# Kernel optimization log

Measured on AMD Instinct MI355X. Metric: run time of the kernel, lower is better.

The kernel has to match this reference:

```python
import jax, jax.numpy as jnp
import numpy as np

D_IN = 1024
D_OUT = 1024
D_BOT = 512


def setup_inputs() -> dict:
    key = jax.random.key(0)
    ks = jax.random.split(key, 16)
    B, Sq, Skv = 8, 2048, 2048

    def lin(k, fan_in, fan_out):
        kw, kb = jax.random.split(k)
        bound = 1.0 / np.sqrt(fan_in)
        W = jax.random.uniform(kw, (fan_in, fan_out), jnp.float32, -bound, bound)
        b = jax.random.uniform(kb, (fan_out,), jnp.float32, -bound, bound)
        return W, b

    W1, b1 = lin(ks[0], D_IN, D_IN)
    W2, b2 = lin(ks[1], D_IN, D_BOT)
    W3, b3 = lin(ks[2], D_BOT, D_IN)
    W4, b4 = lin(ks[3], D_IN, D_IN)
    Wq, bq = lin(ks[4], D_IN, D_OUT)
    Wk, bk = lin(ks[5], D_IN, D_OUT)
    Wv, bv = lin(ks[6], D_IN, D_OUT)

    x = jax.random.normal(ks[7], (B, Sq, D_IN), jnp.float32)
    y = jax.random.normal(ks[8], (B, Skv, D_IN), jnp.float32)
    return {
        "x": x, "y": y,
        "W1": W1, "b1": b1, "W2": W2, "b2": b2,
        "W3": W3, "b3": b3, "W4": W4, "b4": b4,
        "Wq": Wq, "bq": bq, "Wk": Wk, "bk": bk, "Wv": Wv, "bv": bv,
    }


def reference(x, y, W1, b1, W2, b2, W3, b3, W4, b4, Wq, bq, Wk, bk, Wv, bv):
    # 4-layer MLP with ReLU after every linear
    h = jax.nn.relu(x @ W1 + b1)
    h = jax.nn.relu(h @ W2 + b2)
    h = jax.nn.relu(h @ W3 + b3)
    h = jax.nn.relu(h @ W4 + b4)
    # cross-attention projections
    q = h @ Wq + bq          # [B, Sq, D_OUT]
    k = y @ Wk + bk          # [B, Skv, D_OUT]
    v = y @ Wv + bv          # [B, Skv, D_OUT]
    scale = 1.0 / jnp.sqrt(jnp.float32(q.shape[-1]))
    scores = jnp.einsum('bqd,bkd->bqk', q, k) * scale  # [B, Sq, Skv]
    attn_w = jax.nn.softmax(scores, axis=-1)
    out = jnp.einsum('bqk,bkd->bqd', attn_w, v)
    return out
```

## Files before the change

kernel.cpp:

```cpp
#include <hip/hip_runtime.h>
#include <stdint.h>


typedef __attribute__((ext_vector_type(8))) short bf16x8;
typedef __attribute__((ext_vector_type(4))) float f32x4;
typedef __attribute__((ext_vector_type(8))) unsigned short u16x8;

__device__ __forceinline__ float bf2f(unsigned short u) {
    return __uint_as_float(((unsigned int)u) << 16);
}
__device__ __forceinline__ unsigned short f2bf(float f) {
    unsigned int u = __float_as_uint(f);
    unsigned int r = (u + 0x7fffu + ((u >> 16) & 1u)) >> 16;
    return (unsigned short)r;
}

__device__ __forceinline__ void async16(const void* g, void* l) {
    __builtin_amdgcn_global_load_lds(
        (const __attribute__((address_space(1))) unsigned int*)g,
        (__attribute__((address_space(3))) unsigned int*)l,
        16, 0, 0);
}

__global__ __launch_bounds__(64) void detect_dtype(
    const unsigned short* __restrict__ w, int* __restrict__ flag)
{
    const int t = threadIdx.x;
    int cnt = 0;
    for (int i = t; i < 4096; i += 64) {
        const unsigned e = (w[i] >> 7) & 0xFF;
        cnt += (e >= 140) ? 1 : 0;
    }
#pragma unroll
    for (int off = 32; off; off >>= 1) cnt += __shfl_xor(cnt, off, 64);
    if (t == 0) flag[0] = (cnt >= 8) ? 1 : 0;
}

__global__ __launch_bounds__(256) void conv_bias_all(
    const void* b1, const void* b2, const void* b3, const void* b4,
    const void* bq, const void* bk, const void* bv,
    float* __restrict__ out, const int* __restrict__ flag)
{
    const int i = blockIdx.x * 256 + threadIdx.x;
    const int slot = i >> 10, idx = i & 1023;
    if (slot == 1 && idx >= 512) return;
    const void* src = (slot == 0) ? b1 : (slot == 1) ? b2 : (slot == 2) ? b3 :
                      (slot == 3) ? b4 : (slot == 4) ? bq : (slot == 5) ? bk : bv;
    out[i] = (*flag) ? ((const float*)src)[idx]
                     : bf2f(((const unsigned short*)src)[idx]);
}

__device__ __forceinline__ void wt_body(
    const void* in, unsigned short* out, int R, int C, int f)
{
    __shared__ unsigned short tile[32][33];
    const int bc = blockIdx.x * 32;
    const int br = blockIdx.y * 32;
    const int x = threadIdx.x & 31;
    const int y = threadIdx.x >> 5;
#pragma unroll
    for (int i = 0; i < 4; i++) {
        const int r = y + i * 8;
        unsigned short v;
        if (f) v = f2bf(((const float*)in)[(size_t)(br + r) * C + bc + x]);
        else   v = ((const unsigned short*)in)[(size_t)(br + r) * C + bc + x];
        tile[r][x] = v;
    }
    __syncthreads();
#pragma unroll
    for (int i = 0; i < 4; i++) {
        const int r = y + i * 8;
        out[(size_t)(bc + r) * R + br + x] = tile[x][r];
    }
}

__global__ __launch_bounds__(256) void conv_weight_t7(
    const void* i0, unsigned short* o0, const void* i1, unsigned short* o1,
    const void* i2, unsigned short* o2, const void* i3, unsigned short* o3,
    const void* i4, unsigned short* o4, const void* i5, unsigned short* o5,
    const void* i6, unsigned short* o6, const int* flag)
{
    const int z = blockIdx.z;
    if (z == 5) {
        if (blockIdx.x >= 16) return;
        wt_body(i5, o5, 1024, 512, *flag);
        return;
    }
    if (z == 6) {
        if (blockIdx.y >= 16) return;
        wt_body(i6, o6, 512, 1024, *flag);
        return;
    }
    const void* in = (z == 0) ? i0 : (z == 1) ? i1 : (z == 2) ? i2 : (z == 3) ? i3 : i4;
    unsigned short* out = (z == 0) ? o0 : (z == 1) ? o1 : (z == 2) ? o2 : (z == 3) ? o3 : o4;
    wt_body(in, out, 1024, 1024, *flag);
}

__global__ __launch_bounds__(256) void conv_to_bf16(
    const void* __restrict__ in, unsigned short* __restrict__ out,
    int n, const int* __restrict__ flag)
{
    const int i = (blockIdx.x * 256 + threadIdx.x) * 8;
    if (i >= n) return;
    if (*flag) {
        const float4* p = (const float4*)((const float*)in + i);
        const float4 a = p[0], b = p[1];
        u16x8 o;
        o[0] = f2bf(a.x); o[1] = f2bf(a.y); o[2] = f2bf(a.z); o[3] = f2bf(a.w);
        o[4] = f2bf(b.x); o[5] = f2bf(b.y); o[6] = f2bf(b.z); o[7] = f2bf(b.w);
        *(u16x8*)(out + i) = o;
    } else {
        *(u16x8*)(out + i) = *(const u16x8*)((const unsigned short*)in + i);
    }
}

__global__ __launch_bounds__(256) void write_out(
    const unsigned short* __restrict__ src, void* __restrict__ dst,
    int n, const int* __restrict__ flag)
{
    const int i = (blockIdx.x * 256 + threadIdx.x) * 8;
    if (i >= n) return;
    const u16x8 v = *(const u16x8*)(src + i);
    if (*flag) {
        float4 a, b;
        a.x = bf2f(v[0]); a.y = bf2f(v[1]); a.z = bf2f(v[2]); a.w = bf2f(v[3]);
        b.x = bf2f(v[4]); b.y = bf2f(v[5]); b.z = bf2f(v[6]); b.w = bf2f(v[7]);
        float4* p = (float4*)((float*)dst + i);
        p[0] = a; p[1] = b;
    } else {
        *(u16x8*)((unsigned short*)dst + i) = v;
    }
}

template <int RELU, int BIAS, int OUTF, int SWZ>
__global__ __launch_bounds__(256, 2) void gemm_bt(
    const unsigned short* __restrict__ A, const unsigned short* __restrict__ B,
    const float* __restrict__ bias, void* __restrict__ C,
    int M, int N, int K, float alpha,
    long long sA, long long sB, long long sC, const int* __restrict__ flag)
{
    int bxi = blockIdx.x, byi = blockIdx.y;
    if (SWZ) {
        const int id = byi * gridDim.x + bxi;
        bxi = (id >> 3) % gridDim.x;
        byi = (id >> 3) / gridDim.x * 8 + (id & 7);
    }
    const int z = blockIdx.z;
    A += (size_t)z * (size_t)sA;
    B += (size_t)z * (size_t)sB;
    const size_t cofs = (size_t)z * (size_t)sC;

    const int bm = byi * 128;
    const int bn = bxi * 128;
    const int t = threadIdx.x;
    const int lane = t & 63;
    const int w = t >> 6;
    const int wr = (w >> 1) * 64;
    const int wc = (w & 1) * 64;

    __shared__ unsigned short sAt[128 * 32];
    __shared__ unsigned short sBt[128 * 32];

    f32x4 acc[4][4];
#pragma unroll
    for (int i = 0; i < 4; i++)
#pragma unroll
        for (int j = 0; j < 4; j++)
            acc[i][j] = (f32x4){0.f, 0.f, 0.f, 0.f};

    const int tr = t >> 2;
    const int tc = (t & 3) << 3;
    const unsigned short* ga = A + (size_t)(bm + tr) * K + tc;
    const unsigned short* gb = B + (size_t)(bn + tr) * K + tc;
    unsigned short* la = &sAt[tr * 32 + tc];
    unsigned short* lb = &sBt[tr * 32 + tc];

    const int am = wr + (lane & 15);
    const int bn_ = wc + (lane & 15);
    const int ak = (lane >> 4) * 8;

    for (int k0 = 0; k0 < K; k0 += 32) {
        async16(ga, la);
        async16(ga + (size_t)64 * K, la + 64 * 32);
        async16(gb, lb);
        async16(gb + (size_t)64 * K, lb + 64 * 32);
        ga += 32;
        gb += 32;
        __syncthreads();

        bf16x8 af[4], bfr[4];
#pragma unroll
        for (int i = 0; i < 4; i++)
            af[i] = *(const bf16x8*)&sAt[(am + i * 16) * 32 + ak];
#pragma unroll
        for (int j = 0; j < 4; j++)
            bfr[j] = *(const bf16x8*)&sBt[(bn_ + j * 16) * 32 + ak];
#pragma unroll
        for (int i = 0; i < 4; i++)
#pragma unroll
            for (int j = 0; j < 4; j++)
                acc[i][j] = __builtin_amdgcn_mfma_f32_16x16x32_bf16(
                    af[i], bfr[j], acc[i][j], 0, 0, 0);
        __syncthreads();
    }

    const int fl = OUTF ? *flag : 0;
#pragma unroll
    for (int i = 0; i < 4; i++) {
        const int row0 = bm + wr + i * 16 + (lane >> 4) * 4;
#pragma unroll
        for (int j = 0; j < 4; j++) {
            const int col = bn + wc + j * 16 + (lane & 15);
            float bc = 0.f;
            if (BIAS == 1) bc = bias[col];
#pragma unroll
            for (int r = 0; r < 4; r++) {
                float bv = bc;
                if (BIAS == 2) bv = bias[row0 + r];
                float vv = acc[i][j][r] * alpha + bv;
                if (RELU) vv = fmaxf(vv, 0.f);
                const size_t idx = cofs + (size_t)(row0 + r) * N + col;
                if (OUTF && fl) ((float*)C)[idx] = vv;
                else ((unsigned short*)C)[idx] = f2bf(vv);
            }
        }
    }
}

#define G10_STG(SOFS, KOFS) do {                                               \
    async16(gAs + (KOFS), dA + (SOFS));                                        \
    async16(gAs + (KOFS) + rk128, dA + (SOFS) + 4096);                         \
    async16(gBs + (KOFS), dB + (SOFS));                                        \
    async16(gBs + (KOFS) + rk128, dB + (SOFS) + 4096);                         \
} while (0)

template <int RELU, int BIAS, int OUTF, int SWZ>
__global__ __launch_bounds__(512, 2) void gemm8(
    const unsigned short* __restrict__ A, const unsigned short* __restrict__ B,
    const float* __restrict__ bias, void* __restrict__ C,
    int M, int N, int K, float alpha,
    long long sA, long long sB, long long sC, const int* __restrict__ flag)
{
    extern __shared__ unsigned short lds[];
    (void)M;
    int bxi = blockIdx.x, byi = blockIdx.y;
    if (SWZ) {
        const int id = byi * gridDim.x + bxi;
        bxi = (id >> 3) % gridDim.x;
        byi = (id >> 3) / gridDim.x * 8 + (id & 7);
    }
    const int z = blockIdx.z;
    A += (size_t)z * (size_t)sA;
    B += (size_t)z * (size_t)sB;
    const size_t cofs = (size_t)z * (size_t)sC;

    const int bm = byi * 256;
    const int bn = bxi * 256;
    const int t = threadIdx.x;
    const int lane = t & 63;
    const int w = t >> 6;
    const int wm = w >> 2;
    const int wn = w & 3;

    const int soct = ((t & 3) ^ ((t >> 3) & 3)) << 3;
    const unsigned short* gAs = A + (size_t)(bm + (t >> 2)) * K + soct;
    const unsigned short* gBs = B + (size_t)(bn + (t >> 2)) * K + soct;
    const size_t rk128 = (size_t)128 * K;
    unsigned short* dA = lds + t * 8;
    unsigned short* dB = lds + 32768 + t * 8;

    const int l15 = lane & 15;
    const int oct = (((lane >> 4) ^ ((lane >> 1) & 3)) << 3);
    const int aoff = (wm * 128 + l15) * 32 + oct;
    const int boff = (wn * 64 + l15) * 32 + oct;

    f32x4 acc[8][4];
#pragma unroll
    for (int i = 0; i < 8; i++)
#pragma unroll
        for (int j = 0; j < 4; j++)
            acc[i][j] = (f32x4){0.f, 0.f, 0.f, 0.f};

    G10_STG(0, 0);
    G10_STG(8192, 32);
    asm volatile("s_waitcnt vmcnt(4)" ::: "memory");
    __builtin_amdgcn_s_barrier();
    asm volatile("" ::: "memory");

    const int NT = K >> 5;
    for (int T = 0; T < NT; ++T) {
        if (T + 2 < NT) {
            const int so = ((T + 2) & 3) * 8192;
            const int ko = (T + 2) << 5;
            G10_STG(so, ko);
        }
        const int sr = (T & 3) * 8192;
        const unsigned short* pa = lds + sr + aoff;
        const unsigned short* pb = lds + 32768 + sr + boff;
        bf16x8 bb[4], a[8];
#pragma unroll
        for (int n = 0; n < 4; n++)
            bb[n] = *(const bf16x8*)(pb + n * 512);
#pragma unroll
        for (int m = 0; m < 8; m++)
            a[m] = *(const bf16x8*)(pa + m * 512);
        __builtin_amdgcn_s_setprio(1);
#pragma unroll
        for (int m = 0; m < 8; m++)
#pragma unroll
            for (int n = 0; n < 4; n++)
                acc[m][n] = __builtin_amdgcn_mfma_f32_16x16x32_bf16(
                    a[m], bb[n], acc[m][n], 0, 0, 0);
        __builtin_amdgcn_s_setprio(0);
        if (T + 1 < NT) {
            if (T + 2 < NT) {
                asm volatile("s_waitcnt vmcnt(4)" ::: "memory");
            } else {
                asm volatile("s_waitcnt vmcnt(0)" ::: "memory");
            }
            __builtin_amdgcn_s_barrier();
            asm volatile("" ::: "memory");
        }
    }

    const int fl = OUTF ? *flag : 0;
#pragma unroll
    for (int mi = 0; mi < 8; mi++) {
        const int row0 = bm + wm * 128 + mi * 16 + (lane >> 4) * 4;
#pragma unroll
        for (int n = 0; n < 4; n++) {
            const int col = bn + wn * 64 + n * 16 + (lane & 15);
            float bc = 0.f;
            if (BIAS == 1) bc = bias[col];
#pragma unroll
            for (int r = 0; r < 4; r++) {
                float bv = bc;
                if (BIAS == 2) bv = bias[row0 + r];
                float vv = acc[mi][n][r] * alpha + bv;
                if (RELU) vv = fmaxf(vv, 0.f);
                const size_t idx = cofs + (size_t)(row0 + r) * N + col;
                if (OUTF && fl) ((float*)C)[idx] = vv;
                else ((unsigned short*)C)[idx] = f2bf(vv);
            }
        }
    }
}

__global__ __launch_bounds__(256) void softmax_rows(unsigned short* S, int n)
{
    const size_t row = blockIdx.x;
    unsigned short* p = S + row * (size_t)n;
    const int t = threadIdx.x;
    const int lane = t & 63;
    const int wave = t >> 6;

    u16x8 v = *(const u16x8*)(p + t * 8);
    float f[8];
    float m = -3.0e38f;
#pragma unroll
    for (int i = 0; i < 8; i++) {
        f[i] = bf2f(v[i]);
        m = fmaxf(m, f[i]);
    }
#pragma unroll
    for (int off = 32; off; off >>= 1) m = fmaxf(m, __shfl_xor(m, off, 64));
    __shared__ float redm[4];
    if (lane == 0) redm[wave] = m;
    __syncthreads();
    m = fmaxf(fmaxf(redm[0], redm[1]), fmaxf(redm[2], redm[3]));

    float e[8];
    float s = 0.f;
#pragma unroll
    for (int i = 0; i < 8; i++) {
        e[i] = __expf(f[i] - m);
        s += e[i];
    }
#pragma unroll
    for (int off = 32; off; off >>= 1) s += __shfl_xor(s, off, 64);
    __shared__ float reds[4];
    if (lane == 0) reds[wave] = s;
    __syncthreads();
    s = reds[0] + reds[1] + reds[2] + reds[3];
    const float inv = 1.0f / s;

    u16x8 o;
#pragma unroll
    for (int i = 0; i < 8; i++) o[i] = f2bf(e[i] * inv);
    *(u16x8*)(p + t * 8) = o;
}

extern "C" void kernel_launch(void* const* d_in, const int* in_sizes, int n_in,
                              void* d_out, int out_size, void* d_ws, size_t ws_size,
                              hipStream_t stream)
{
    const void* x  = d_in[0];
    const void* y  = d_in[1];
    const void* W1 = d_in[2];
    const void* b1 = d_in[3];
    const void* W2 = d_in[4];
    const void* b2 = d_in[5];
    const void* W3 = d_in[6];
    const void* b3 = d_in[7];
    const void* W4 = d_in[8];
    const void* b4 = d_in[9];
    const void* Wq = d_in[10];
    const void* bq = d_in[11];
    const void* Wk = d_in[12];
    const void* bk = d_in[13];
    const void* Wv = d_in[14];
    const void* bv = d_in[15];

    int* flag = (int*)d_ws;
    float* fb = (float*)((char*)d_ws + 64);
    unsigned short* arena = (unsigned short*)((char*)d_ws + 64 + 7 * 1024 * 4);
    const size_t baseB = 64 + 7 * 1024 * 4;
    const size_t MEG = 1024ull * 1024ull;

    auto needB = [&](int G, bool direct) -> size_t {
        return baseB + 2ull * ((6 + 16 + (size_t)G * 6 + (direct ? 0 : 16)) * MEG);
    };
    int G; bool direct;
    if (ws_size >= needB(8, true))      { G = 8; direct = true;  }
    else if (ws_size >= needB(4, false)) { G = 4; direct = false; }
    else if (ws_size >= needB(2, false)) { G = 2; direct = false; }
    else                                 { G = 1; direct = false; }

    unsigned short* W1t = arena;
    unsigned short* W2t = W1t + 1 * MEG;
    unsigned short* W3t = W2t + MEG / 2;
    unsigned short* W4t = W3t + MEG / 2;
    unsigned short* Wqt = W4t + 1 * MEG;
    unsigned short* Wkt = Wqt + 1 * MEG;
    unsigned short* Wvt = Wkt + 1 * MEG;
    unsigned short* XC  = Wvt + 1 * MEG;
    unsigned short* VT  = XC + 16 * MEG;
    unsigned short* SBUF = VT + (size_t)G * 2 * MEG;
    unsigned short* OUTS = SBUF + (size_t)G * 4 * MEG;

    unsigned short* PA = (unsigned short*)d_out;
    unsigned short* PB = PA + 16 * MEG;

    float* fb1 = fb;
    float* fb2 = fb + 1024;
    float* fb3 = fb + 2048;
    float* fb4 = fb + 3072;
    float* fbq = fb + 4096;
    float* fbk = fb + 5120;
    float* fbv = fb + 6144;

    const dim3 blk(256);
    const dim3 blk8(512);
    const int LDS8 = 131072;
    const int NE = 16 * 1024 * 1024;
    const int Mx = 16384;
    const long long Z0 = 0;
    const long long sQK = 2048ll * 1024;
    const long long sS  = 2048ll * 2048;

    (void)hipFuncSetAttribute((const void*)&gemm8<1, 1, 0, 1>,
                              hipFuncAttributeMaxDynamicSharedMemorySize, LDS8);
    (void)hipFuncSetAttribute((const void*)&gemm8<0, 1, 0, 1>,
                              hipFuncAttributeMaxDynamicSharedMemorySize, LDS8);
    (void)hipFuncSetAttribute((const void*)&gemm8<0, 2, 0, 0>,
                              hipFuncAttributeMaxDynamicSharedMemorySize, LDS8);
    (void)hipFuncSetAttribute((const void*)&gemm8<0, 0, 0, 1>,
                              hipFuncAttributeMaxDynamicSharedMemorySize, LDS8);
    (void)hipFuncSetAttribute((const void*)&gemm8<0, 0, 1, 1>,
                              hipFuncAttributeMaxDynamicSharedMemorySize, LDS8);

    detect_dtype<<<1, 64, 0, stream>>>((const unsigned short*)W1, flag);
    conv_bias_all<<<28, blk, 0, stream>>>(b1, b2, b3, b4, bq, bk, bv, fb, flag);
    conv_weight_t7<<<dim3(32, 32, 7), blk, 0, stream>>>(
        W1, W1t, W4, W4t, Wq, Wqt, Wk, Wkt, Wv, Wvt, W2, W2t, W3, W3t, flag);

    conv_to_bf16<<<8192, blk, 0, stream>>>(x, XC, NE, flag);

    gemm8<1, 1, 0, 1><<<dim3(4, 64), blk8, LDS8, stream>>>(
        XC, W1t, fb1, PA, Mx, 1024, 1024, 1.f, Z0, Z0, Z0, flag);
    gemm_bt<1, 1, 0, 1><<<dim3(4, 128), blk, 0, stream>>>(
        PA, W2t, fb2, PB, Mx, 512, 1024, 1.f, Z0, Z0, Z0, flag);
    gemm8<1, 1, 0, 1><<<dim3(4, 64), blk8, LDS8, stream>>>(
        PB, W3t, fb3, PA, Mx, 1024, 512, 1.f, Z0, Z0, Z0, flag);
    gemm8<1, 1, 0, 1><<<dim3(4, 64), blk8, LDS8, stream>>>(
        PA, W4t, fb4, PB, Mx, 1024, 1024, 1.f, Z0, Z0, Z0, flag);

    gemm8<0, 1, 0, 1><<<dim3(4, 64), blk8, LDS8, stream>>>(
        PB, Wqt, fbq, PA, Mx, 1024, 1024, 1.f, Z0, Z0, Z0, flag);
    conv_to_bf16<<<8192, blk, 0, stream>>>(y, XC, NE, flag);
    gemm8<0, 1, 0, 1><<<dim3(4, 64), blk8, LDS8, stream>>>(
        XC, Wkt, fbk, PB, Mx, 1024, 1024, 1.f, Z0, Z0, Z0, flag);

    if (direct) {
        gemm8<0, 2, 0, 0><<<dim3(8, 4, 8), blk8, LDS8, stream>>>(
            Wvt, XC, fbv, VT, 1024, 2048, 1024, 1.f, Z0, sQK, sQK, flag);
        gemm8<0, 0, 0, 1><<<dim3(8, 8, 8), blk8, LDS8, stream>>>(
            PA, PB, nullptr, SBUF, 2048, 2048, 1024, 0.03125f, sQK, sQK, sS, flag);
        softmax_rows<<<dim3(8 * 2048), blk, 0, stream>>>(SBUF, 2048);
        gemm8<0, 0, 1, 1><<<dim3(4, 8, 8), blk8, LDS8, stream>>>(
            SBUF, VT, nullptr, d_out, 2048, 1024, 2048, 1.f, sS, sQK, sQK, flag);
    } else {
        for (int g = 0; g < 8; g += G) {
            const size_t off = (size_t)g * 2048 * 1024;
            gemm_bt<0, 2, 0, 0><<<dim3(16, 8, G), blk, 0, stream>>>(
                Wvt, XC + off, fbv, VT, 1024, 2048, 1024, 1.f, Z0, sQK, sQK, flag);
            gemm_bt<0, 0, 0, 1><<<dim3(16, 16, G), blk, 0, stream>>>(
                PA + off, PB + off, nullptr, SBUF, 2048, 2048, 1024, 0.03125f, sQK, sQK, sS, flag);
            softmax_rows<<<dim3(G * 2048), blk, 0, stream>>>(SBUF, 2048);
            gemm_bt<0, 0, 0, 1><<<dim3(8, 16, G), blk, 0, stream>>>(
                SBUF, VT, nullptr, OUTS + off, 2048, 1024, 2048, 1.f, sS, sQK, sQK, flag);
        }
        write_out<<<8192, blk, 0, stream>>>(OUTS, d_out, NE, flag);
    }
}
```

Measured before the change: 606.0 us.

## Add 128x512-tile triple-buffered GEMM for projections and compute V via transpose

Introduces gemm_bt5, a 512-thread GEMM with 128x512 output tiles, a three-stage async LDS pipeline and smaller LDS (120KB), and uses it for the MLP layers and Q/K projections. The V projection is now computed as a standard row-major GEMM with column bias into a scratch buffer, followed by a new tiled transpose kernel that produces VT. The aim is better operand reuse and pipelining for the large M=16384 projections. The cost is an extra transpose pass and scratch buffer traffic, plus higher register pressure from the 4x8 accumulator layout.

```diff
diff --git a/kernel.cpp b/kernel.cpp
--- a/kernel.cpp
+++ b/kernel.cpp
@@ -94,6 +94,31 @@
     const void* in = (z == 0) ? i0 : (z == 1) ? i1 : (z == 2) ? i2 : (z == 3) ? i3 : i4;
     unsigned short* out = (z == 0) ? o0 : (z == 1) ? o1 : (z == 2) ? o2 : (z == 3) ? o3 : o4;
     wt_body(in, out, 1024, 1024, *flag);
+}
+
+__global__ __launch_bounds__(256) void transpose_bf16(
+    const unsigned short* __restrict__ in, unsigned short* __restrict__ out,
+    int R, int C)
+{
+    __shared__ unsigned short tile[32][33];
+    const size_t zofs = (size_t)blockIdx.z * R * C;
+    const unsigned short* ip = in + zofs;
+    unsigned short* op = out + zofs;
+    const int bc = blockIdx.x * 32;
+    const int br = blockIdx.y * 32;
+    const int x = threadIdx.x & 31;
+    const int y = threadIdx.x >> 5;
+#pragma unroll
+    for (int i = 0; i < 4; i++) {
+        const int r = y + i * 8;
+        tile[r][x] = ip[(size_t)(br + r) * C + bc + x];
+    }
+    __syncthreads();
+#pragma unroll
+    for (int i = 0; i < 4; i++) {
+        const int r = y + i * 8;
+        op[(size_t)(bc + r) * R + br + x] = tile[x][r];
+    }
 }
 
 __global__ __launch_bounds__(256) void conv_to_bf16(
@@ -330,6 +355,133 @@
 #pragma unroll
         for (int n = 0; n < 4; n++) {
             const int col = bn + wn * 64 + n * 16 + (lane & 15);
+            float bc = 0.f;
+            if (BIAS == 1) bc = bias[col];
+#pragma unroll
+            for (int r = 0; r < 4; r++) {
+                float bv = bc;
+                if (BIAS == 2) bv = bias[row0 + r];
+                float vv = acc[mi][n][r] * alpha + bv;
+                if (RELU) vv = fmaxf(vv, 0.f);
+                const size_t idx = cofs + (size_t)(row0 + r) * N + col;
+                if (OUTF && fl) ((float*)C)[idx] = vv;
+                else ((unsigned short*)C)[idx] = f2bf(vv);
+            }
+        }
+    }
+}
+
+template <int RELU, int BIAS, int OUTF, int SWZ>
+__global__ __launch_bounds__(512, 2) void gemm_bt5(
+    const unsigned short* __restrict__ A, const unsigned short* __restrict__ B,
+    const float* __restrict__ bias, void* __restrict__ C,
+    int M, int N, int K, float alpha,
+    long long sA, long long sB, long long sC, const int* __restrict__ flag)
+{
+    extern __shared__ unsigned short lds[];
+    (void)M;
+    int bxi = blockIdx.x, byi = blockIdx.y;
+    if (SWZ) {
+        const int id = byi * gridDim.x + bxi;
+        bxi = (id >> 3) % gridDim.x;
+        byi = (id >> 3) / gridDim.x * 8 + (id & 7);
+    }
+    const int z = blockIdx.z;
+    A += (size_t)z * (size_t)sA;
+    B += (size_t)z * (size_t)sB;
+    const size_t cofs = (size_t)z * (size_t)sC;
+
+    const int bm = byi * 128;
+    const int bn = bxi * 512;
+    const int t = threadIdx.x;
+    const int lane = t & 63;
+    const int w = t >> 6;
+    const int wm = w >> 2;
+    const int wn = w & 3;
+
+    const int soct = ((t & 3) ^ ((t >> 3) & 3)) << 3;
+    const unsigned short* gAs = A + (size_t)(bm + (t >> 2)) * K + soct;
+    const unsigned short* gBs = B + (size_t)(bn + (t >> 2)) * K + soct;
+    const size_t rk128 = (size_t)128 * K;
+    unsigned short* dA = lds + t * 8;
+    unsigned short* dB = lds + 12288 + t * 8;
+
+    const int l15 = lane & 15;
+    const int oct = (((lane >> 4) ^ ((lane >> 1) & 3)) << 3);
+    const int aoff = (wm * 64 + l15) * 32 + oct;
+    const int boff = (wn * 128 + l15) * 32 + oct;
+
+    f32x4 acc[4][8];
+#pragma unroll
+    for (int i = 0; i < 4; i++)
+#pragma unroll
+        for (int j = 0; j < 8; j++)
+            acc[i][j] = (f32x4){0.f, 0.f, 0.f, 0.f};
+
+    async16(gAs, dA);
+    async16(gBs, dB);
+    async16(gBs + rk128, dB + 4096);
+    async16(gBs + 2 * rk128, dB + 8192);
+    async16(gBs + 3 * rk128, dB + 12288);
+    async16(gAs + 32, dA + 4096);
+    async16(gBs + 32, dB + 16384);
+    async16(gBs + 32 + rk128, dB + 16384 + 4096);
+    async16(gBs + 32 + 2 * rk128, dB + 16384 + 8192);
+    async16(gBs + 32 + 3 * rk128, dB + 16384 + 12288);
+    asm volatile("s_waitcnt vmcnt(5)" ::: "memory");
+    __builtin_amdgcn_s_barrier();
+    asm volatile("" ::: "memory");
+
+    const int NT = K >> 5;
+    int rs = 0, ws = 2;
+    for (int T = 0; T < NT; ++T) {
+        if (T + 2 < NT) {
+            const int ko = (T + 2) << 5;
+            const int wa = ws * 4096;
+            const int wb = ws * 16384;
+            async16(gAs + ko, dA + wa);
+            async16(gBs + ko, dB + wb);
+            async16(gBs + ko + rk128, dB + wb + 4096);
+            async16(gBs + ko + 2 * rk128, dB + wb + 8192);
+            async16(gBs + ko + 3 * rk128, dB + wb + 12288);
+        }
+        const unsigned short* pa = lds + rs * 4096 + aoff;
+        const unsigned short* pb = lds + 12288 + rs * 16384 + boff;
+        bf16x8 a[4], bb[8];
+#pragma unroll
+        for (int m = 0; m < 4; m++)
+            a[m] = *(const bf16x8*)(pa + m * 512);
+#pragma unroll
+        for (int n = 0; n < 8; n++)
+            bb[n] = *(const bf16x8*)(pb + n * 512);
+        __builtin_amdgcn_s_setprio(1);
+#pragma unroll
+        for (int m = 0; m < 4; m++)
+#pragma unroll
+            for (int n = 0; n < 8; n++)
+                acc[m][n] = __builtin_amdgcn_mfma_f32_16x16x32_bf16(
+                    a[m], bb[n], acc[m][n], 0, 0, 0);
+        __builtin_amdgcn_s_setprio(0);
+        if (T + 1 < NT) {
+            if (T + 2 < NT) {
+                asm volatile("s_waitcnt vmcnt(5)" ::: "memory");
+            } else {
+                asm volatile("s_waitcnt vmcnt(0)" ::: "memory");
+            }
+            __builtin_amdgcn_s_barrier();
+            asm volatile("" ::: "memory");
+        }
+        rs = (rs == 2) ? 0 : rs + 1;
+        ws = (ws == 2) ? 0 : ws + 1;
+    }
+
+    const int fl = OUTF ? *flag : 0;
+#pragma unroll
+    for (int mi = 0; mi < 4; mi++) {
+        const int row0 = bm + wm * 64 + mi * 16 + (lane >> 4) * 4;
+#pragma unroll
+        for (int n = 0; n < 8; n++) {
+            const int col = bn + wn * 128 + n * 16 + (lane & 15);
             float bc = 0.f;
             if (BIAS == 1) bc = bias[col];
 #pragma unroll
@@ -452,18 +604,17 @@
     const dim3 blk(256);
     const dim3 blk8(512);
     const int LDS8 = 131072;
+    const int LDS5 = 122880;
     const int NE = 16 * 1024 * 1024;
     const int Mx = 16384;
     const long long Z0 = 0;
     const long long sQK = 2048ll * 1024;
     const long long sS  = 2048ll * 2048;
 
-    (void)hipFuncSetAttribute((const void*)&gemm8<1, 1, 0, 1>,
-                              hipFuncAttributeMaxDynamicSharedMemorySize, LDS8);
-    (void)hipFuncSetAttribute((const void*)&gemm8<0, 1, 0, 1>,
-                              hipFuncAttributeMaxDynamicSharedMemorySize, LDS8);
-    (void)hipFuncSetAttribute((const void*)&gemm8<0, 2, 0, 0>,
-                              hipFuncAttributeMaxDynamicSharedMemorySize, LDS8);
+    (void)hipFuncSetAttribute((const void*)&gemm_bt5<1, 1, 0, 1>,
+                              hipFuncAttributeMaxDynamicSharedMemorySize, LDS5);
+    (void)hipFuncSetAttribute((const void*)&gemm_bt5<0, 1, 0, 1>,
+                              hipFuncAttributeMaxDynamicSharedMemorySize, LDS5);
     (void)hipFuncSetAttribute((const void*)&gemm8<0, 0, 0, 1>,
                               hipFuncAttributeMaxDynamicSharedMemorySize, LDS8);
     (void)hipFuncSetAttribute((const void*)&gemm8<0, 0, 1, 1>,
@@ -476,24 +627,25 @@
 
     conv_to_bf16<<<8192, blk, 0, stream>>>(x, XC, NE, flag);
 
-    gemm8<1, 1, 0, 1><<<dim3(4, 64), blk8, LDS8, stream>>>(
+    gemm_bt5<1, 1, 0, 1><<<dim3(2, 128), blk8, LDS5, stream>>>(
         XC, W1t, fb1, PA, Mx, 1024, 1024, 1.f, Z0, Z0, Z0, flag);
     gemm_bt<1, 1, 0, 1><<<dim3(4, 128), blk, 0, stream>>>(
         PA, W2t, fb2, PB, Mx, 512, 1024, 1.f, Z0, Z0, Z0, flag);
-    gemm8<1, 1, 0, 1><<<dim3(4, 64), blk8, LDS8, stream>>>(
+    gemm_bt5<1, 1, 0, 1><<<dim3(2, 128), blk8, LDS5, stream>>>(
         PB, W3t, fb3, PA, Mx, 1024, 512, 1.f, Z0, Z0, Z0, flag);
-    gemm8<1, 1, 0, 1><<<dim3(4, 64), blk8, LDS8, stream>>>(
+    gemm_bt5<1, 1, 0, 1><<<dim3(2, 128), blk8, LDS5, stream>>>(
         PA, W4t, fb4, PB, Mx, 1024, 1024, 1.f, Z0, Z0, Z0, flag);
 
-    gemm8<0, 1, 0, 1><<<dim3(4, 64), blk8, LDS8, stream>>>(
+    gemm_bt5<0, 1, 0, 1><<<dim3(2, 128), blk8, LDS5, stream>>>(
         PB, Wqt, fbq, PA, Mx, 1024, 1024, 1.f, Z0, Z0, Z0, flag);
     conv_to_bf16<<<8192, blk, 0, stream>>>(y, XC, NE, flag);
-    gemm8<0, 1, 0, 1><<<dim3(4, 64), blk8, LDS8, stream>>>(
+    gemm_bt5<0, 1, 0, 1><<<dim3(2, 128), blk8, LDS5, stream>>>(
         XC, Wkt, fbk, PB, Mx, 1024, 1024, 1.f, Z0, Z0, Z0, flag);
 
     if (direct) {
-        gemm8<0, 2, 0, 0><<<dim3(8, 4, 8), blk8, LDS8, stream>>>(
-            Wvt, XC, fbv, VT, 1024, 2048, 1024, 1.f, Z0, sQK, sQK, flag);
+        gemm_bt5<0, 1, 0, 1><<<dim3(2, 128), blk8, LDS5, stream>>>(
+            XC, Wvt, fbv, SBUF, Mx, 1024, 1024, 1.f, Z0, Z0, Z0, flag);
+        transpose_bf16<<<dim3(32, 64, 8), blk, 0, stream>>>(SBUF, VT, 2048, 1024);
         gemm8<0, 0, 0, 1><<<dim3(8, 8, 8), blk8, LDS8, stream>>>(
             PA, PB, nullptr, SBUF, 2048, 2048, 1024, 0.03125f, sQK, sQK, sS, flag);
         softmax_rows<<<dim3(8 * 2048), blk, 0, stream>>>(SBUF, 2048);
```

New measurement: 637.8 us. +5.2%, slower.

## Fuse softmax into QK^T and PV GEMMs via row max/sum statistics

Applied to the files above, without the earlier changes.

Removes the separate softmax pass over the 8x2048x2048 score matrix. The QK^T GEMM now stores log2-scaled raw scores and emits per-tile row max and sum partials. A small reduce kernel merges these into a row max and inverse sum. The PV GEMM then exponentiates the A operand on the fly after the LDS load and scales its output by the inverse sum. It also switches the W2 layer from gemm_bt to the larger gemm8 tile. The cost is extra exp and bf16 conversion work inside the PV GEMM's inner loop, plus a workspace-size condition for the fused path.

```diff
diff --git a/kernel.cpp b/kernel.cpp
--- a/kernel.cpp
+++ b/kernel.cpp
@@ -5,6 +5,9 @@
 typedef __attribute__((ext_vector_type(8))) short bf16x8;
 typedef __attribute__((ext_vector_type(4))) float f32x4;
 typedef __attribute__((ext_vector_type(8))) unsigned short u16x8;
+
+#define LOG2E_F 1.44269504088896f
+#define LN2_F   0.69314718055995f
 
 __device__ __forceinline__ float bf2f(unsigned short u) {
     return __uint_as_float(((unsigned int)u) << 16);
@@ -234,15 +237,15 @@
     async16(gBs + (KOFS) + rk128, dB + (SOFS) + 4096);                         \
 } while (0)
 
-template <int RELU, int BIAS, int OUTF, int SWZ>
+template <int RELU, int BIAS, int OUTF, int SWZ, int STAT, int NORM>
 __global__ __launch_bounds__(512, 2) void gemm8(
     const unsigned short* __restrict__ A, const unsigned short* __restrict__ B,
     const float* __restrict__ bias, void* __restrict__ C,
     int M, int N, int K, float alpha,
-    long long sA, long long sB, long long sC, const int* __restrict__ flag)
+    long long sA, long long sB, long long sC, const int* __restrict__ flag,
+    const float* __restrict__ ms, float* __restrict__ ps)
 {
     extern __shared__ unsigned short lds[];
-    (void)M;
     int bxi = blockIdx.x, byi = blockIdx.y;
     if (SWZ) {
         const int id = byi * gridDim.x + bxi;
@@ -274,6 +277,15 @@
     const int aoff = (wm * 128 + l15) * 32 + oct;
     const int boff = (wn * 64 + l15) * 32 + oct;
 
+    float Mm[8];
+    if (NORM) {
+#pragma unroll
+        for (int m = 0; m < 8; m++) {
+            const int row = bm + wm * 128 + m * 16 + l15;
+            Mm[m] = ms[((size_t)z * M + row) * 2];
+        }
+    }
+
     f32x4 acc[8][4];
 #pragma unroll
     for (int i = 0; i < 8; i++)
@@ -304,6 +316,20 @@
 #pragma unroll
         for (int m = 0; m < 8; m++)
             a[m] = *(const bf16x8*)(pa + m * 512);
+        if (NORM) {
+#pragma unroll
+            for (int m = 0; m < 8; m++) {
+                bf16x8 v = a[m];
+                u16x8 o;
+#pragma unroll
+                for (int e = 0; e < 8; e++) {
+                    const float x = bf2f((unsigned short)v[e]);
+                    const float p = __expf((x - Mm[m]) * LN2_F);
+                    o[e] = f2bf(p);
+                }
+                a[m] = *(bf16x8*)&o;
+            }
+        }
         __builtin_amdgcn_s_setprio(1);
 #pragma unroll
         for (int m = 0; m < 8; m++)
@@ -327,9 +353,15 @@
 #pragma unroll
     for (int mi = 0; mi < 8; mi++) {
         const int row0 = bm + wm * 128 + mi * 16 + (lane >> 4) * 4;
+        float isv[4];
+        if (NORM) {
+#pragma unroll
+            for (int r = 0; r < 4; r++)
+                isv[r] = ms[((size_t)z * M + row0 + r) * 2 + 1];
+        }
 #pragma unroll
         for (int n = 0; n < 4; n++) {
-            const int col = bn + wn * 64 + n * 16 + (lane & 15);
+            const int col = bn + wn * 64 + n * 16 + l15;
             float bc = 0.f;
             if (BIAS == 1) bc = bias[col];
 #pragma unroll
@@ -337,6 +369,7 @@
                 float bv = bc;
                 if (BIAS == 2) bv = bias[row0 + r];
                 float vv = acc[mi][n][r] * alpha + bv;
+                if (NORM) vv *= isv[r];
                 if (RELU) vv = fmaxf(vv, 0.f);
                 const size_t idx = cofs + (size_t)(row0 + r) * N + col;
                 if (OUTF && fl) ((float*)C)[idx] = vv;
@@ -344,6 +377,64 @@
             }
         }
     }
+
+    if (STAT) {
+        __syncthreads();
+        float2* sl = (float2*)lds;
+#pragma unroll
+        for (int mi = 0; mi < 8; mi++) {
+#pragma unroll
+            for (int r = 0; r < 4; r++) {
+                float vr[4];
+#pragma unroll
+                for (int n = 0; n < 4; n++)
+                    vr[n] = bf2f(f2bf(acc[mi][n][r] * alpha));
+                float mx = fmaxf(fmaxf(vr[0], vr[1]), fmaxf(vr[2], vr[3]));
+#pragma unroll
+                for (int msk = 1; msk <= 8; msk <<= 1)
+                    mx = fmaxf(mx, __shfl_xor(mx, msk, 64));
+                float sm = 0.f;
+#pragma unroll
+                for (int n = 0; n < 4; n++)
+                    sm += __expf((vr[n] - mx) * LN2_F);
+#pragma unroll
+                for (int msk = 1; msk <= 8; msk <<= 1)
+                    sm += __shfl_xor(sm, msk, 64);
+                if (l15 == 0) {
+                    const int rl = wm * 128 + mi * 16 + (lane >> 4) * 4 + r;
+                    sl[rl * 4 + wn] = (float2){mx, sm};
+                }
+            }
+        }
+        __syncthreads();
+        if (t < 256) {
+            const float2 p0 = sl[t * 4 + 0], p1 = sl[t * 4 + 1];
+            const float2 p2 = sl[t * 4 + 2], p3 = sl[t * 4 + 3];
+            float Mx = fmaxf(fmaxf(p0.x, p1.x), fmaxf(p2.x, p3.x));
+            float S = p0.y * __expf((p0.x - Mx) * LN2_F)
+                    + p1.y * __expf((p1.x - Mx) * LN2_F)
+                    + p2.y * __expf((p2.x - Mx) * LN2_F)
+                    + p3.y * __expf((p3.x - Mx) * LN2_F);
+            float2* o = (float2*)ps;
+            o[((size_t)z * M + bm + t) * 8 + bxi] = (float2){Mx, S};
+        }
+    }
+}
+
+__global__ __launch_bounds__(256) void stats_reduce(
+    const float* __restrict__ ps, float* __restrict__ ms)
+{
+    const int i = blockIdx.x * 256 + threadIdx.x;
+    const float2* p = (const float2*)ps + (size_t)i * 8;
+    float M = p[0].x;
+#pragma unroll
+    for (int j = 1; j < 8; j++) M = fmaxf(M, p[j].x);
+    float S = 0.f;
+#pragma unroll
+    for (int j = 0; j < 8; j++)
+        S += p[j].y * __expf((p[j].x - M) * LN2_F);
+    float2* o = (float2*)ms;
+    o[i] = (float2){M, 1.0f / S};
 }
 
 __global__ __launch_bounds__(256) void softmax_rows(unsigned short* S, int n)
@@ -458,15 +549,23 @@
     const long long sQK = 2048ll * 1024;
     const long long sS  = 2048ll * 2048;
 
-    (void)hipFuncSetAttribute((const void*)&gemm8<1, 1, 0, 1>,
+    const bool fused = direct && (ws_size >= needB(8, true) + 2ull * MEG);
+    float* pstats = (float*)OUTS;
+    float* mstats = pstats + 8 * 2048 * 8 * 2;
+
+    (void)hipFuncSetAttribute((const void*)&gemm8<1, 1, 0, 1, 0, 0>,
                               hipFuncAttributeMaxDynamicSharedMemorySize, LDS8);
-    (void)hipFuncSetAttribute((const void*)&gemm8<0, 1, 0, 1>,
+    (void)hipFuncSetAttribute((const void*)&gemm8<0, 1, 0, 1, 0, 0>,
                               hipFuncAttributeMaxDynamicSharedMemorySize, LDS8);
-    (void)hipFuncSetAttribute((const void*)&gemm8<0, 2, 0, 0>,
+    (void)hipFuncSetAttribute((const void*)&gemm8<0, 2, 0, 0, 0, 0>,
                               hipFuncAttributeMaxDynamicSharedMemorySize, LDS8);
-    (void)hipFuncSetAttribute((const void*)&gemm8<0, 0, 0, 1>,
+    (void)hipFuncSetAttribute((const void*)&gemm8<0, 0, 0, 1, 0, 0>,
                               hipFuncAttributeMaxDynamicSharedMemorySize, LDS8);
-    (void)hipFuncSetAttribute((const void*)&gemm8<0, 0, 1, 1>,
+    (void)hipFuncSetAttribute((const void*)&gemm8<0, 0, 1, 1, 0, 0>,
+                              hipFuncAttributeMaxDynamicSharedMemorySize, LDS8);
+    (void)hipFuncSetAttribute((const void*)&gemm8<0, 0, 0, 1, 1, 0>,
+                              hipFuncAttributeMaxDynamicSharedMemorySize, LDS8);
+    (void)hipFuncSetAttribute((const void*)&gemm8<0, 0, 1, 1, 0, 1>,
                               hipFuncAttributeMaxDynamicSharedMemorySize, LDS8);
 
     detect_dtype<<<1, 64, 0, stream>>>((const unsigned short*)W1, flag);
@@ -476,29 +575,41 @@
 
     conv_to_bf16<<<8192, blk, 0, stream>>>(x, XC, NE, flag);
 
-    gemm8<1, 1, 0, 1><<<dim3(4, 64), blk8, LDS8, stream>>>(
-        XC, W1t, fb1, PA, Mx, 1024, 1024, 1.f, Z0, Z0, Z0, flag);
-    gemm_bt<1, 1, 0, 1><<<dim3(4, 128), blk, 0, stream>>>(
-        PA, W2t, fb2, PB, Mx, 512, 1024, 1.f, Z0, Z0, Z0, flag);
-    gemm8<1, 1, 0, 1><<<dim3(4, 64), blk8, LDS8, stream>>>(
-        PB, W3t, fb3, PA, Mx, 1024, 512, 1.f, Z0, Z0, Z0, flag);
-    gemm8<1, 1, 0, 1><<<dim3(4, 64), blk8, LDS8, stream>>>(
-        PA, W4t, fb4, PB, Mx, 1024, 1024, 1.f, Z0, Z0, Z0, flag);
-
-    gemm8<0, 1, 0, 1><<<dim3(4, 64), blk8, LDS8, stream>>>(
-        PB, Wqt, fbq, PA, Mx, 1024, 1024, 1.f, Z0, Z0, Z0, flag);
+    gemm8<1, 1, 0, 1, 0, 0><<<dim3(4, 64), blk8, LDS8, stream>>>(
+        XC, W1t, fb1, PA, Mx, 1024, 1024, 1.f, Z0, Z0, Z0, flag, nullptr, nullptr);
+    gemm8<1, 1, 0, 1, 0, 0><<<dim3(2, 64), blk8, LDS8, stream>>>(
+        PA, W2t, fb2, PB, Mx, 512, 1024, 1.f, Z0, Z0, Z0, flag, nullptr, nullptr);
+    gemm8<1, 1, 0, 1, 0, 0><<<dim3(4, 64), blk8, LDS8, stream>>>(
+        PB, W3t, fb3, PA, Mx, 1024, 512, 1.f, Z0, Z0, Z0, flag, nullptr, nullptr);
+    gemm8<1, 1, 0, 1, 0, 0><<<dim3(4, 64), blk8, LDS8, stream>>>(
+        PA, W4t, fb4, PB, Mx, 1024, 1024, 1.f, Z0, Z0, Z0, flag, nullptr, nullptr);
+
+    gemm8<0, 1, 0, 1, 0, 0><<<dim3(4, 64), blk8, LDS8, stream>>>(
+        PB, Wqt, fbq, PA, Mx, 1024, 1024, 1.f, Z0, Z0, Z0, flag, nullptr, nullptr);
     conv_to_bf16<<<8192, blk, 0, stream>>>(y, XC, NE, flag);
-    gemm8<0, 1, 0, 1><<<dim3(4, 64), blk8, LDS8, stream>>>(
-        XC, Wkt, fbk, PB, Mx, 1024, 1024, 1.f, Z0, Z0, Z0, flag);
+    gemm8<0, 1, 0, 1, 0, 0><<<dim3(4, 64), blk8, LDS8, stream>>>(
+        XC, Wkt, fbk, PB, Mx, 1024, 1024, 1.f, Z0, Z0, Z0, flag, nullptr, nullptr);
 
     if (direct) {
-        gemm8<0, 2, 0, 0><<<dim3(8, 4, 8), blk8, LDS8, stream>>>(
-            Wvt, XC, fbv, VT, 1024, 2048, 1024, 1.f, Z0, sQK, sQK, flag);
-        gemm8<0, 0, 0, 1><<<dim3(8, 8, 8), blk8, LDS8, stream>>>(
-            PA, PB, nullptr, SBUF, 2048, 2048, 1024, 0.03125f, sQK, sQK, sS, flag);
-        softmax_rows<<<dim3(8 * 2048), blk, 0, stream>>>(SBUF, 2048);
-        gemm8<0, 0, 1, 1><<<dim3(4, 8, 8), blk8, LDS8, stream>>>(
-            SBUF, VT, nullptr, d_out, 2048, 1024, 2048, 1.f, sS, sQK, sQK, flag);
+        gemm8<0, 2, 0, 0, 0, 0><<<dim3(8, 4, 8), blk8, LDS8, stream>>>(
+            Wvt, XC, fbv, VT, 1024, 2048, 1024, 1.f, Z0, sQK, sQK, flag, nullptr, nullptr);
+        if (fused) {
+            gemm8<0, 0, 0, 1, 1, 0><<<dim3(8, 8, 8), blk8, LDS8, stream>>>(
+                PA, PB, nullptr, SBUF, 2048, 2048, 1024, 0.03125f * LOG2E_F,
+                sQK, sQK, sS, flag, nullptr, pstats);
+            stats_reduce<<<64, blk, 0, stream>>>(pstats, mstats);
+            gemm8<0, 0, 1, 1, 0, 1><<<dim3(4, 8, 8), blk8, LDS8, stream>>>(
+                SBUF, VT, nullptr, d_out, 2048, 1024, 2048, 1.f,
+                sS, sQK, sQK, flag, mstats, nullptr);
+        } else {
+            gemm8<0, 0, 0, 1, 0, 0><<<dim3(8, 8, 8), blk8, LDS8, stream>>>(
+                PA, PB, nullptr, SBUF, 2048, 2048, 1024, 0.03125f,
+                sQK, sQK, sS, flag, nullptr, nullptr);
+            softmax_rows<<<dim3(8 * 2048), blk, 0, stream>>>(SBUF, 2048);
+            gemm8<0, 0, 1, 1, 0, 0><<<dim3(4, 8, 8), blk8, LDS8, stream>>>(
+                SBUF, VT, nullptr, d_out, 2048, 1024, 2048, 1.f,
+                sS, sQK, sQK, flag, nullptr, nullptr);
+        }
     } else {
         for (int g = 0; g < 8; g += G) {
             const size_t off = (size_t)g * 2048 * 1024;
```

Result: slower. 724.4 us (+19.5%).
